# Optimization experiments

Measured on AMD Instinct MI355X. Metric: run time of the kernel, lower is better.

## Reference

```python
import jax, jax.numpy as jnp
import numpy as np

N, E, B = 50000, 400000, 128
F_IN, EDIM, EMB, H = 64, 8, 64, 4
HC = EMB * H  # 256
L = 3          # gnn_layers
DN = 256       # dense_neurons
NEG_SLOPE = 0.2
EPS = 1e-5


def setup_inputs():
    key = jax.random.key(0)
    ks = jax.random.split(key, 32)
    s = 0.05
    d = {}
    d["x"] = jax.random.normal(ks[0], (N, F_IN), jnp.float32)
    d["edge_index"] = jax.random.randint(ks[1], (2, E), 0, N, jnp.int32)
    d["edge_attr"] = jax.random.normal(ks[2], (E, EDIM), jnp.float32)
    d["mol_formal_charge"] = jax.random.normal(ks[3], (B,), jnp.float32)
    d["mol_nrot"] = jax.random.normal(ks[4], (B,), jnp.float32)
    d["batch_index"] = jnp.sort(jax.random.randint(ks[5], (N,), 0, B, jnp.int32))
    # GATv2 params, stacked over L layers (in_dim == EMB == F_IN for all layers)
    d["gat_Wl"] = jax.random.normal(ks[6], (L, F_IN, HC), jnp.float32) * s
    d["gat_Wr"] = jax.random.normal(ks[7], (L, F_IN, HC), jnp.float32) * s
    d["gat_We"] = jax.random.normal(ks[8], (L, EDIM, HC), jnp.float32) * s
    d["gat_att"] = jax.random.normal(ks[9], (L, H, EMB), jnp.float32) * s
    d["gat_b"] = jnp.zeros((L, HC), jnp.float32)
    d["tr_W"] = jax.random.normal(ks[10], (L, HC, EMB), jnp.float32) * s
    d["tr_b"] = jnp.zeros((L, EMB), jnp.float32)
    d["bn_g"] = jnp.ones((L, EMB), jnp.float32)
    d["bn_b"] = jnp.zeros((L, EMB), jnp.float32)
    d["gate_W"] = jax.random.normal(ks[11], (EMB, 1), jnp.float32) * s
    d["gate_b"] = jnp.zeros((1,), jnp.float32)
    d["lin1_W"] = jax.random.normal(ks[12], (EMB + 2, DN), jnp.float32) * s
    d["lin1_b"] = jnp.zeros((DN,), jnp.float32)
    d["fc1_W"] = jax.random.normal(ks[13], (DN, DN // 2), jnp.float32) * s
    d["fc1_b"] = jnp.zeros((DN // 2,), jnp.float32)
    d["fc2_W"] = jax.random.normal(ks[14], (DN // 2, DN // 4), jnp.float32) * s
    d["fc2_b"] = jnp.zeros((DN // 4,), jnp.float32)
    d["out_W"] = jax.random.normal(ks[15], (DN // 4, 1), jnp.float32) * s
    d["out_b"] = jnp.zeros((1,), jnp.float32)
    return d


def _seg_softmax(logits, seg, num):
    # numerically stable per-segment softmax over leading axis
    mx = jax.ops.segment_max(logits, seg, num_segments=num)
    ex = jnp.exp(logits - mx[seg])
    den = jax.ops.segment_sum(ex, seg, num_segments=num)
    return ex / den[seg]


def reference(x, edge_index, edge_attr, mol_formal_charge, mol_nrot, batch_index,
              gat_Wl, gat_Wr, gat_We, gat_att, gat_b, tr_W, tr_b, bn_g, bn_b,
              gate_W, gate_b, lin1_W, lin1_b, fc1_W, fc1_b, fc2_W, fc2_b,
              out_W, out_b):
    src, dst = edge_index[0], edge_index[1]  # messages flow src -> dst
    h = x
    for l in range(L):
        xl = (h @ gat_Wl[l]).reshape(N, H, EMB)
        xr = (h @ gat_Wr[l]).reshape(N, H, EMB)
        ea = (edge_attr @ gat_We[l]).reshape(E, H, EMB)
        xls = xl[src]                                   # [E,H,C]
        m = jax.nn.leaky_relu(xls + xr[dst] + ea, NEG_SLOPE)
        logit = jnp.einsum('ehc,hc->eh', m, gat_att[l])  # [E,H]
        alpha = _seg_softmax(logit, dst, N)              # [E,H]
        agg = jax.ops.segment_sum(alpha[:, :, None] * xls, dst, num_segments=N)
        h = agg.reshape(N, HC) + gat_b[l]
        h = jax.nn.relu(h @ tr_W[l] + tr_b[l])
        # BatchNorm1d (training-mode batch stats, biased var)
        mu = h.mean(0)
        var = h.var(0)
        h = (h - mu) / jnp.sqrt(var + EPS) * bn_g[l] + bn_b[l]
    # AttentionalAggregation pooling
    gate = h @ gate_W + gate_b                           # [N,1]
    w = _seg_softmax(gate, batch_index, B)
    pooled = jax.ops.segment_sum(w * h, batch_index, num_segments=B)  # [B,EMB]
    z = jnp.concatenate([pooled, mol_formal_charge[:, None], mol_nrot[:, None]], axis=1)
    z = jax.nn.relu(z @ lin1_W + lin1_b)
    z = jax.nn.relu(z @ fc1_W + fc1_b)
    z = jax.nn.relu(z @ fc2_W + fc2_b)
    return z @ out_W + out_b                             # [B,1]
```

## Files before the change

kernel.cpp:

```cpp
#include <hip/hip_runtime.h>

#define NN 50000
#define NE 400000
#define NB 128
#define NINF (-__builtin_inff())

__device__ __forceinline__ float dpp_add16(float x) {
    int v = __float_as_int(x);
    x += __int_as_float(__builtin_amdgcn_update_dpp(0, v, 0xB1, 0xF, 0xF, true));
    v = __float_as_int(x);
    x += __int_as_float(__builtin_amdgcn_update_dpp(0, v, 0x4E, 0xF, 0xF, true));
    v = __float_as_int(x);
    x += __int_as_float(__builtin_amdgcn_update_dpp(0, v, 0x141, 0xF, 0xF, true));
    v = __float_as_int(x);
    x += __int_as_float(__builtin_amdgcn_update_dpp(0, v, 0x140, 0xF, 0xF, true));
    return x;
}

__global__ __launch_bounds__(256) void k_hist(const int* __restrict__ dstv, int* __restrict__ deg) {
    int e = blockIdx.x * 256 + threadIdx.x;
    if (e < NE) atomicAdd(&deg[dstv[e]], 1);
}

__global__ __launch_bounds__(1024) void k_scan(const int* __restrict__ deg, int* __restrict__ rowptr) {
    __shared__ int wsum[16];
    __shared__ int total_s;
    const int tid = threadIdx.x, lane = tid & 63, w = tid >> 6;
    if (tid == 0) rowptr[0] = 0;
    int carry = 0;
    for (int base = 0; base < NN; base += 1024) {
        int i = base + tid;
        int v = (i < NN) ? deg[i] : 0;
        int incl = v;
        #pragma unroll
        for (int off = 1; off < 64; off <<= 1) {
            int t = __shfl_up(incl, off);
            if (lane >= off) incl += t;
        }
        if (lane == 63) wsum[w] = incl;
        __syncthreads();
        if (tid < 16) {
            int s = wsum[tid];
            int si = s;
            #pragma unroll
            for (int off = 1; off < 16; off <<= 1) {
                int t = __shfl_up(si, off, 16);
                if (tid >= off) si += t;
            }
            wsum[tid] = si - s;
            if (tid == 15) total_s = si;
        }
        __syncthreads();
        if (i < NN) rowptr[i + 1] = carry + wsum[w] + incl;
        carry += total_s;
        __syncthreads();
    }
}

__global__ __launch_bounds__(256) void k_scatter(const int* __restrict__ dstv, const int* __restrict__ srcv,
                                                 const float* __restrict__ eattr, const int* __restrict__ rowptr,
                                                 int* __restrict__ cnt, int* __restrict__ eid,
                                                 int* __restrict__ src_perm, float4* __restrict__ ea_perm,
                                                 int use_perm) {
    int e = blockIdx.x * 256 + threadIdx.x;
    if (e < NE) {
        int d = dstv[e];
        int pos = rowptr[d] + atomicAdd(&cnt[d], 1);
        eid[pos] = e;
        if (use_perm) {
            src_perm[pos] = srcv[e];
            ea_perm[(size_t)pos * 2] = ((const float4*)eattr)[e * 2];
            ea_perm[(size_t)pos * 2 + 1] = ((const float4*)eattr)[e * 2 + 1];
        }
    }
}

__global__ __launch_bounds__(256) void k_gemm64(const float* __restrict__ A, const float* __restrict__ Wl,
                                                const float* __restrict__ Wr, float* __restrict__ Cl,
                                                float* __restrict__ Cr, const float* __restrict__ stats,
                                                const float* __restrict__ bg, const float* __restrict__ bb) {
    __shared__ float As[64 * 64];
    __shared__ float Ws[64 * 128];
    __shared__ float sc_s[64], sh_s[64], shW_s[128];
    const int tid = threadIdx.x;
    const int mat = blockIdx.y >> 1, ch = blockIdx.y & 1;
    const float* W = mat ? Wr : Wl;
    float* C = mat ? Cr : Cl;
    const int r0b = blockIdx.x * 64;

    if (stats) {
        if (tid < 64) {
            const float mu = stats[tid] * (1.0f / (float)NN);
            const float var = stats[64 + tid] * (1.0f / (float)NN) - mu * mu;
            const float rstd = rsqrtf(var + 1e-5f);
            const float sc = bg[tid] * rstd;
            sc_s[tid] = sc;
            sh_s[tid] = fmaf(-mu, sc, bb[tid]);
        }
        __syncthreads();
    }
    for (int i = tid; i < 2048; i += 256) {
        const int k = i >> 5, c4 = i & 31;
        float4 v = ((const float4*)W)[k * 64 + ch * 32 + c4];
        if (stats) {
            const float s = sc_s[k];
            v.x *= s; v.y *= s; v.z *= s; v.w *= s;
        }
        ((float4*)Ws)[i] = v;
    }
    for (int i = tid; i < 1024; i += 256) {
        const int r = i >> 4, c4 = i & 15;
        const int rg = (r0b + r < NN) ? (r0b + r) : (NN - 1);
        ((float4*)As)[i] = ((const float4*)A)[rg * 16 + c4];
    }
    if (stats && tid < 128) {
        const float* wc = W + ch * 128 + tid;
        float s = 0.f;
        for (int k = 0; k < 64; ++k) s = fmaf(sh_s[k], wc[k * 256], s);
        shW_s[tid] = s;
    }
    __syncthreads();

    const int cg = tid & 31;
    const int rq = tid >> 5;
    float acc[8][4];
    if (stats) {
        #pragma unroll
        for (int rr = 0; rr < 8; ++rr) {
            acc[rr][0] = shW_s[cg * 4]; acc[rr][1] = shW_s[cg * 4 + 1];
            acc[rr][2] = shW_s[cg * 4 + 2]; acc[rr][3] = shW_s[cg * 4 + 3];
        }
    } else {
        #pragma unroll
        for (int rr = 0; rr < 8; ++rr)
            acc[rr][0] = acc[rr][1] = acc[rr][2] = acc[rr][3] = 0.f;
    }

    for (int kq = 0; kq < 16; ++kq) {
        float4 av[8];
        #pragma unroll
        for (int rr = 0; rr < 8; ++rr)
            av[rr] = ((const float4*)As)[(rq * 8 + rr) * 16 + kq];
        #pragma unroll
        for (int kk = 0; kk < 4; ++kk) {
            const float4 w = *(const float4*)(Ws + ((kq * 4 + kk) << 7) + (cg << 2));
            #pragma unroll
            for (int rr = 0; rr < 8; ++rr) {
                const float a = reinterpret_cast<const float*>(&av[rr])[kk];
                acc[rr][0] = fmaf(a, w.x, acc[rr][0]);
                acc[rr][1] = fmaf(a, w.y, acc[rr][1]);
                acc[rr][2] = fmaf(a, w.z, acc[rr][2]);
                acc[rr][3] = fmaf(a, w.w, acc[rr][3]);
            }
        }
    }
    #pragma unroll
    for (int rr = 0; rr < 8; ++rr) {
        const int r = r0b + rq * 8 + rr;
        if (r < NN)
            *(float4*)(C + (size_t)r * 256 + ch * 128 + cg * 4) =
                make_float4(acc[rr][0], acc[rr][1], acc[rr][2], acc[rr][3]);
    }
}

template <bool PERM>
__global__ __launch_bounds__(256, 4) void k_agg(const float* __restrict__ xl, float* __restrict__ xragg,
                                                const float* __restrict__ att, const float* __restrict__ gatb,
                                                const int* __restrict__ rowptr, const int* __restrict__ eid,
                                                const int* __restrict__ srcv, const float* __restrict__ eattr,
                                                const int* __restrict__ src_perm, const float4* __restrict__ ea_perm,
                                                const float* __restrict__ We) {
    const int lane = threadIdx.x & 63;
    const float4 we0 = ((const float4*)(We + 0 * 256))[lane];
    const float4 we1 = ((const float4*)(We + 1 * 256))[lane];
    const float4 we2 = ((const float4*)(We + 2 * 256))[lane];
    const float4 we3 = ((const float4*)(We + 3 * 256))[lane];
    const float4 we4 = ((const float4*)(We + 4 * 256))[lane];
    const float4 we5 = ((const float4*)(We + 5 * 256))[lane];
    const float4 we6 = ((const float4*)(We + 6 * 256))[lane];
    const float4 we7 = ((const float4*)(We + 7 * 256))[lane];
    const float4 attf = ((const float4*)att)[lane];
    const float4 gbf = ((const float4*)gatb)[lane];
    const int nw = gridDim.x * (blockDim.x >> 6);
    int wid = blockIdx.x * (blockDim.x >> 6) + (threadIdx.x >> 6);

#define LOADE(X, idx)                                                          \
    {                                                                          \
        int s_;                                                                \
        const float4* eap_;                                                    \
        if (PERM) {                                                            \
            s_ = src_perm[idx];                                                \
            eap_ = ea_perm + (size_t)(idx) * 2;                                \
        } else {                                                               \
            const int e_ = eid[idx];                                           \
            s_ = srcv[e_];                                                     \
            eap_ = (const float4*)(eattr + (size_t)e_ * 8);                    \
        }                                                                      \
        X##x = ((const float4*)(xl + (size_t)s_ * 256))[lane];                 \
        X##a = eap_[0];                                                        \
        X##b = eap_[1];                                                        \
    }

#define PROC(X)                                                                \
    {                                                                          \
        float v0 = fmaf(X##a.x, we0.x, xr.x), v1 = fmaf(X##a.x, we0.y, xr.y);  \
        float v2 = fmaf(X##a.x, we0.z, xr.z), v3 = fmaf(X##a.x, we0.w, xr.w);  \
        v0 = fmaf(X##a.y, we1.x, v0); v1 = fmaf(X##a.y, we1.y, v1);            \
        v2 = fmaf(X##a.y, we1.z, v2); v3 = fmaf(X##a.y, we1.w, v3);            \
        v0 = fmaf(X##a.z, we2.x, v0); v1 = fmaf(X##a.z, we2.y, v1);            \
        v2 = fmaf(X##a.z, we2.z, v2); v3 = fmaf(X##a.z, we2.w, v3);            \
        v0 = fmaf(X##a.w, we3.x, v0); v1 = fmaf(X##a.w, we3.y, v1);            \
        v2 = fmaf(X##a.w, we3.z, v2); v3 = fmaf(X##a.w, we3.w, v3);            \
        v0 = fmaf(X##b.x, we4.x, v0); v1 = fmaf(X##b.x, we4.y, v1);            \
        v2 = fmaf(X##b.x, we4.z, v2); v3 = fmaf(X##b.x, we4.w, v3);            \
        v0 = fmaf(X##b.y, we5.x, v0); v1 = fmaf(X##b.y, we5.y, v1);            \
        v2 = fmaf(X##b.y, we5.z, v2); v3 = fmaf(X##b.y, we5.w, v3);            \
        v0 = fmaf(X##b.z, we6.x, v0); v1 = fmaf(X##b.z, we6.y, v1);            \
        v2 = fmaf(X##b.z, we6.z, v2); v3 = fmaf(X##b.z, we6.w, v3);            \
        v0 = fmaf(X##b.w, we7.x, v0); v1 = fmaf(X##b.w, we7.y, v1);            \
        v2 = fmaf(X##b.w, we7.z, v2); v3 = fmaf(X##b.w, we7.w, v3);            \
        v0 += X##x.x; v1 += X##x.y; v2 += X##x.z; v3 += X##x.w;                \
        v0 = fmaxf(v0, 0.2f * v0); v1 = fmaxf(v1, 0.2f * v1);                  \
        v2 = fmaxf(v2, 0.2f * v2); v3 = fmaxf(v3, 0.2f * v3);                  \
        float part = v0 * attf.x;                                              \
        part = fmaf(v1, attf.y, part);                                         \
        part = fmaf(v2, attf.z, part);                                         \
        part = fmaf(v3, attf.w, part);                                         \
        part = dpp_add16(part);                                                \
        const float p = __expf(part);                                          \
        den += p;                                                              \
        c0 = fmaf(p, X##x.x, c0);                                              \
        c1 = fmaf(p, X##x.y, c1);                                              \
        c2 = fmaf(p, X##x.z, c2);                                              \
        c3 = fmaf(p, X##x.w, c3);                                              \
    }

    for (int n = wid; n < NN; n += nw) {
        const int e0 = rowptr[n], e1 = rowptr[n + 1];
        const float4 xr = ((const float4*)(xragg + (size_t)n * 256))[lane];
        float den = 0.f, c0 = 0.f, c1 = 0.f, c2 = 0.f, c3 = 0.f;
        float4 Ax, Aa, Ab, Bx, Ba, Bb;
        const int cnt = e1 - e0;
        if (cnt > 0) {
            LOADE(A, e0);
            if (cnt > 1) {
                LOADE(B, e0 + 1);
                int i = e0;
                for (; i + 3 < e1; i += 2) {
                    PROC(A);
                    LOADE(A, i + 2);
                    PROC(B);
                    LOADE(B, i + 3);
                }
                const int r = e1 - i;
                PROC(A);
                if (r == 3) {
                    LOADE(A, i + 2);
                    PROC(B);
                    PROC(A);
                } else {
                    PROC(B);
                }
            } else {
                PROC(A);
            }
        }
        float4 o;
        if (cnt > 0) {
            const float inv = 1.0f / den;
            o.x = fmaf(c0, inv, gbf.x);
            o.y = fmaf(c1, inv, gbf.y);
            o.z = fmaf(c2, inv, gbf.z);
            o.w = fmaf(c3, inv, gbf.w);
        } else {
            o = gbf;
        }
        ((float4*)(xragg + (size_t)n * 256))[lane] = o;
    }
#undef LOADE
#undef PROC
}

__global__ __launch_bounds__(256) void k_tr(const float* __restrict__ A, const float* __restrict__ W,
                                            const float* __restrict__ bias, float* __restrict__ Hout,
                                            float* __restrict__ stats) {
    __shared__ float As[64 * 68];
    __shared__ float Ws[64 * 64];
    __shared__ float red[128];
    const int tid = threadIdx.x;
    const int cg = tid & 15;
    const int rq = tid >> 4;
    const int r0b = blockIdx.x * 64;

    float acc[4][4];
    {
        const float b0 = bias[cg * 4], b1 = bias[cg * 4 + 1], b2 = bias[cg * 4 + 2], b3 = bias[cg * 4 + 3];
        #pragma unroll
        for (int rr = 0; rr < 4; ++rr) { acc[rr][0] = b0; acc[rr][1] = b1; acc[rr][2] = b2; acc[rr][3] = b3; }
    }

    for (int kc = 0; kc < 4; ++kc) {
        if (kc) __syncthreads();
        for (int i = tid; i < 1024; i += 256)
            ((float4*)Ws)[i] = ((const float4*)(W + kc * 4096))[i];
        for (int i = tid; i < 1024; i += 256) {
            const int r = i >> 4, c4 = i & 15;
            const int rg = (r0b + r < NN) ? (r0b + r) : (NN - 1);
            *(float4*)(As + r * 68 + c4 * 4) = ((const float4*)A)[(size_t)rg * 64 + kc * 16 + c4];
        }
        __syncthreads();
        for (int kq = 0; kq < 16; ++kq) {
            float4 av[4];
            #pragma unroll
            for (int rr = 0; rr < 4; ++rr)
                av[rr] = *(const float4*)(As + (rq * 4 + rr) * 68 + kq * 4);
            #pragma unroll
            for (int kk = 0; kk < 4; ++kk) {
                const float4 w = *(const float4*)(Ws + ((kq * 4 + kk) << 6) + (cg << 2));
                #pragma unroll
                for (int rr = 0; rr < 4; ++rr) {
                    const float a = reinterpret_cast<const float*>(&av[rr])[kk];
                    acc[rr][0] = fmaf(a, w.x, acc[rr][0]);
                    acc[rr][1] = fmaf(a, w.y, acc[rr][1]);
                    acc[rr][2] = fmaf(a, w.z, acc[rr][2]);
                    acc[rr][3] = fmaf(a, w.w, acc[rr][3]);
                }
            }
        }
    }
    float lsum[4] = {0.f, 0.f, 0.f, 0.f}, lsq[4] = {0.f, 0.f, 0.f, 0.f};
    #pragma unroll
    for (int rr = 0; rr < 4; ++rr) {
        const int r = r0b + rq * 4 + rr;
        if (r < NN) {
            float v0 = fmaxf(acc[rr][0], 0.f), v1 = fmaxf(acc[rr][1], 0.f);
            float v2 = fmaxf(acc[rr][2], 0.f), v3 = fmaxf(acc[rr][3], 0.f);
            lsum[0] += v0; lsum[1] += v1; lsum[2] += v2; lsum[3] += v3;
            lsq[0] = fmaf(v0, v0, lsq[0]); lsq[1] = fmaf(v1, v1, lsq[1]);
            lsq[2] = fmaf(v2, v2, lsq[2]); lsq[3] = fmaf(v3, v3, lsq[3]);
            *(float4*)(Hout + (size_t)r * 64 + cg * 4) = make_float4(v0, v1, v2, v3);
        }
    }
    __syncthreads();
    if (tid < 128) red[tid] = 0.f;
    __syncthreads();
    #pragma unroll
    for (int j = 0; j < 4; ++j) {
        atomicAdd(&red[cg * 4 + j], lsum[j]);
        atomicAdd(&red[64 + cg * 4 + j], lsq[j]);
    }
    __syncthreads();
    if (tid < 64) {
        atomicAdd(&stats[tid], red[tid]);
        atomicAdd(&stats[64 + tid], red[64 + tid]);
    }
}

__global__ __launch_bounds__(256) void k_poolhead(const float* __restrict__ h, const float* __restrict__ gw,
                                                  const int* __restrict__ bidx, const float* __restrict__ stats,
                                                  const float* __restrict__ bg, const float* __restrict__ bb,
                                                  const float* __restrict__ fc, const float* __restrict__ nrot,
                                                  const float* __restrict__ W1, const float* __restrict__ b1,
                                                  const float* __restrict__ W2, const float* __restrict__ b2,
                                                  const float* __restrict__ W3, const float* __restrict__ b3,
                                                  const float* __restrict__ W4, const float* __restrict__ b4,
                                                  float* __restrict__ out) {
    __shared__ float gate_s[1024];
    __shared__ float red[4];
    __shared__ float pp[4][64];
    __shared__ float scb[64], shb[64];
    __shared__ float z[66], a1[256], a2[128], a3[64];
    const int b = blockIdx.x, tid = threadIdx.x, lane = tid & 63, w = tid >> 6;
    if (tid < 64) {
        const float mu = stats[tid] * (1.0f / (float)NN);
        const float var = stats[64 + tid] * (1.0f / (float)NN) - mu * mu;
        const float rstd = rsqrtf(var + 1e-5f);
        const float sc = bg[tid] * rstd;
        scb[tid] = sc;
        shb[tid] = fmaf(-mu, sc, bb[tid]);
    }
    int lo = 0, hi = NN;
    while (lo < hi) { int mid = (lo + hi) >> 1; if (bidx[mid] < b) lo = mid + 1; else hi = mid; }
    const int s0 = lo;
    lo = 0; hi = NN;
    while (lo < hi) { int mid = (lo + hi) >> 1; if (bidx[mid] < b + 1) lo = mid + 1; else hi = mid; }
    const int s1 = lo;
    const int seg = s1 - s0;
    __syncthreads();

    const float gwv = gw[lane] * scb[lane];
    for (int i = s0 + w; i < s1; i += 4) {
        float p = h[(size_t)i * 64 + lane] * gwv;
        #pragma unroll
        for (int off = 32; off; off >>= 1) p += __shfl_xor(p, off);
        if (lane == 0) gate_s[i - s0] = p;
    }
    __syncthreads();
    float v = NINF;
    for (int i = tid; i < seg; i += 256) v = fmaxf(v, gate_s[i]);
    #pragma unroll
    for (int off = 32; off; off >>= 1) v = fmaxf(v, __shfl_xor(v, off));
    if (lane == 0) red[w] = v;
    __syncthreads();
    const float mx = fmaxf(fmaxf(red[0], red[1]), fmaxf(red[2], red[3]));
    __syncthreads();
    float d = 0.f;
    for (int i = tid; i < seg; i += 256) {
        const float ex = __expf(gate_s[i] - mx);
        gate_s[i] = ex;
        d += ex;
    }
    #pragma unroll
    for (int off = 32; off; off >>= 1) d += __shfl_xor(d, off);
    if (lane == 0) red[w] = d;
    __syncthreads();
    const float den = red[0] + red[1] + red[2] + red[3];
    const int c = tid & 63, ro = tid >> 6;
    float acc = 0.f;
    for (int i = s0 + ro; i < s1; i += 4) acc = fmaf(gate_s[i - s0], h[(size_t)i * 64 + c], acc);
    pp[ro][c] = acc;
    __syncthreads();
    if (tid < 64) {
        const float raw = (pp[0][tid] + pp[1][tid] + pp[2][tid] + pp[3][tid]) / den;
        z[tid] = (seg > 0) ? fmaf(raw, scb[tid], shb[tid]) : shb[tid];
    }
    if (tid == 64) z[64] = fc[b];
    if (tid == 65) z[65] = nrot[b];
    __syncthreads();
    float s = b1[tid];
    for (int k = 0; k < 66; ++k) s = fmaf(z[k], W1[k * 256 + tid], s);
    a1[tid] = fmaxf(s, 0.f);
    __syncthreads();
    if (tid < 128) {
        float s2 = b2[tid];
        for (int k = 0; k < 256; ++k) s2 = fmaf(a1[k], W2[k * 128 + tid], s2);
        a2[tid] = fmaxf(s2, 0.f);
    }
    __syncthreads();
    if (tid < 64) {
        float s3 = b3[tid];
        for (int k = 0; k < 128; ++k) s3 = fmaf(a2[k], W3[k * 64 + tid], s3);
        a3[tid] = fmaxf(s3, 0.f);
    }
    __syncthreads();
    if (tid < 64) {
        float p = a3[tid] * W4[tid];
        #pragma unroll
        for (int off = 32; off; off >>= 1) p += __shfl_xor(p, off);
        if (tid == 0) out[b] = p + b4[0];
    }
}

extern "C" void kernel_launch(void* const* d_in, const int* in_sizes, int n_in,
                              void* d_out, int out_size, void* d_ws, size_t ws_size,
                              hipStream_t stream) {
    const float* x     = (const float*)d_in[0];
    const int*   ei    = (const int*)d_in[1];
    const float* eattr = (const float*)d_in[2];
    const float* fcv   = (const float*)d_in[3];
    const float* nrot  = (const float*)d_in[4];
    const int*   bidx  = (const int*)d_in[5];
    const float* Wl    = (const float*)d_in[6];
    const float* Wr    = (const float*)d_in[7];
    const float* We    = (const float*)d_in[8];
    const float* att   = (const float*)d_in[9];
    const float* gatb  = (const float*)d_in[10];
    const float* trW   = (const float*)d_in[11];
    const float* trb   = (const float*)d_in[12];
    const float* bng   = (const float*)d_in[13];
    const float* bnb   = (const float*)d_in[14];
    const float* gateW = (const float*)d_in[15];
    const float* W1    = (const float*)d_in[17];
    const float* b1    = (const float*)d_in[18];
    const float* W2    = (const float*)d_in[19];
    const float* b2    = (const float*)d_in[20];
    const float* W3    = (const float*)d_in[21];
    const float* b3    = (const float*)d_in[22];
    const float* W4    = (const float*)d_in[23];
    const float* b4    = (const float*)d_in[24];
    float* out = (float*)d_out;

    const int* srcv = ei;
    const int* dstv = ei + NE;

    char* w = (char*)d_ws;
    float*  xl       = (float*)(w);
    float*  xragg    = (float*)(w + 51200000);
    float*  hbuf     = (float*)(w + 102400000);
    int*    deg      = (int*)  (w + 102400000);
    int*    cnt      = (int*)  (w + 102600000);
    int*    eid      = (int*)  (w + 115200000);
    int*    rowptr   = (int*)  (w + 116800000);
    float*  stats    = (float*)(w + 117000064);
    int*    src_perm = (int*)  (w + 117042048);
    float4* ea_perm  = (float4*)(w + 118642048);
    const bool use_perm = (ws_size >= (size_t)131442048);

    hipMemsetAsync(deg, 0, 400000, stream);
    hipMemsetAsync(stats, 0, 1536, stream);
    k_hist<<<(NE + 255) / 256, 256, 0, stream>>>(dstv, deg);
    k_scan<<<1, 1024, 0, stream>>>(deg, rowptr);
    k_scatter<<<(NE + 255) / 256, 256, 0, stream>>>(dstv, srcv, eattr, rowptr, cnt, eid,
                                                    src_perm, ea_perm, use_perm ? 1 : 0);

    const float* hin = x;
    for (int l = 0; l < 3; ++l) {
        const float* st = (l == 0) ? nullptr : (stats + (l - 1) * 128);
        const float* g  = (l == 0) ? nullptr : (bng + (l - 1) * 64);
        const float* bb = (l == 0) ? nullptr : (bnb + (l - 1) * 64);
        dim3 gg((NN + 63) / 64, 4);
        k_gemm64<<<gg, 256, 0, stream>>>(hin, Wl + l * 16384, Wr + l * 16384, xl, xragg, st, g, bb);
        if (use_perm)
            k_agg<true><<<2048, 256, 0, stream>>>(xl, xragg, att + l * 256, gatb + l * 256, rowptr,
                                                  eid, srcv, eattr, src_perm, ea_perm, We + l * 2048);
        else
            k_agg<false><<<2048, 256, 0, stream>>>(xl, xragg, att + l * 256, gatb + l * 256, rowptr,
                                                   eid, srcv, eattr, src_perm, ea_perm, We + l * 2048);
        k_tr<<<(NN + 63) / 64, 256, 0, stream>>>(xragg, trW + l * 16384, trb + l * 64, hbuf, stats + l * 128);
        hin = hbuf;
    }
    k_poolhead<<<NB, 256, 0, stream>>>(hbuf, gateW, bidx, stats + 2 * 128, bng + 128, bnb + 128,
                                       fcv, nrot, W1, b1, W2, b2, W3, b3, W4, b4, out);
}
```

Measured before the change: 759.5 us.

## Parallelize degree scan and enlarge GEMM register tiles with transposed LDS

```diff
diff --git a/kernel.cpp b/kernel.cpp
--- a/kernel.cpp
+++ b/kernel.cpp
@@ -22,39 +22,53 @@
     if (e < NE) atomicAdd(&deg[dstv[e]], 1);
 }
 
-__global__ __launch_bounds__(1024) void k_scan(const int* __restrict__ deg, int* __restrict__ rowptr) {
-    __shared__ int wsum[16];
-    __shared__ int total_s;
+__global__ __launch_bounds__(256) void k_scan1(const int* __restrict__ deg, int* __restrict__ bsum) {
+    __shared__ int ws[4];
     const int tid = threadIdx.x, lane = tid & 63, w = tid >> 6;
-    if (tid == 0) rowptr[0] = 0;
-    int carry = 0;
-    for (int base = 0; base < NN; base += 1024) {
-        int i = base + tid;
-        int v = (i < NN) ? deg[i] : 0;
-        int incl = v;
-        #pragma unroll
-        for (int off = 1; off < 64; off <<= 1) {
-            int t = __shfl_up(incl, off);
-            if (lane >= off) incl += t;
-        }
-        if (lane == 63) wsum[w] = incl;
-        __syncthreads();
-        if (tid < 16) {
-            int s = wsum[tid];
-            int si = s;
-            #pragma unroll
-            for (int off = 1; off < 16; off <<= 1) {
-                int t = __shfl_up(si, off, 16);
-                if (tid >= off) si += t;
-            }
-            wsum[tid] = si - s;
-            if (tid == 15) total_s = si;
-        }
-        __syncthreads();
-        if (i < NN) rowptr[i + 1] = carry + wsum[w] + incl;
-        carry += total_s;
-        __syncthreads();
-    }
+    const int i = blockIdx.x * 256 + tid;
+    int v = (i < NN) ? deg[i] : 0;
+    #pragma unroll
+    for (int off = 32; off; off >>= 1) v += __shfl_xor(v, off);
+    if (lane == 0) ws[w] = v;
+    __syncthreads();
+    if (tid == 0) bsum[blockIdx.x] = ws[0] + ws[1] + ws[2] + ws[3];
+}
+
+__global__ __launch_bounds__(256) void k_scan2(const int* __restrict__ bsum, int* __restrict__ boff, int nblk) {
+    __shared__ int ws[4];
+    const int tid = threadIdx.x, lane = tid & 63, w = tid >> 6;
+    int v = (tid < nblk) ? bsum[tid] : 0;
+    int incl = v;
+    #pragma unroll
+    for (int off = 1; off < 64; off <<= 1) {
+        int t = __shfl_up(incl, off);
+        if (lane >= off) incl += t;
+    }
+    if (lane == 63) ws[w] = incl;
+    __syncthreads();
+    int add = 0;
+    for (int k = 0; k < w; ++k) add += ws[k];
+    if (tid < nblk) boff[tid] = add + incl - v;
+}
+
+__global__ __launch_bounds__(256) void k_scan3(const int* __restrict__ deg, const int* __restrict__ boff,
+                                               int* __restrict__ rowptr) {
+    __shared__ int ws[4];
+    const int tid = threadIdx.x, lane = tid & 63, w = tid >> 6;
+    const int i = blockIdx.x * 256 + tid;
+    int v = (i < NN) ? deg[i] : 0;
+    int incl = v;
+    #pragma unroll
+    for (int off = 1; off < 64; off <<= 1) {
+        int t = __shfl_up(incl, off);
+        if (lane >= off) incl += t;
+    }
+    if (lane == 63) ws[w] = incl;
+    __syncthreads();
+    int add = boff[blockIdx.x];
+    for (int k = 0; k < w; ++k) add += ws[k];
+    if (i < NN) rowptr[i + 1] = add + incl;
+    if (i == 0) rowptr[0] = 0;
 }
 
 __global__ __launch_bounds__(256) void k_scatter(const int* __restrict__ dstv, const int* __restrict__ srcv,
@@ -79,14 +93,14 @@
                                                 const float* __restrict__ Wr, float* __restrict__ Cl,
                                                 float* __restrict__ Cr, const float* __restrict__ stats,
                                                 const float* __restrict__ bg, const float* __restrict__ bb) {
-    __shared__ float As[64 * 64];
+    __shared__ float At[64 * 132];
     __shared__ float Ws[64 * 128];
     __shared__ float sc_s[64], sh_s[64], shW_s[128];
     const int tid = threadIdx.x;
     const int mat = blockIdx.y >> 1, ch = blockIdx.y & 1;
     const float* W = mat ? Wr : Wl;
     float* C = mat ? Cr : Cl;
-    const int r0b = blockIdx.x * 64;
+    const int r0b = blockIdx.x * 128;
 
     if (stats) {
         if (tid < 64) {
@@ -108,10 +122,14 @@
         }
         ((float4*)Ws)[i] = v;
     }
-    for (int i = tid; i < 1024; i += 256) {
-        const int r = i >> 4, c4 = i & 15;
+    for (int i = tid; i < 2048; i += 256) {
+        const int r = i >> 4, kq = i & 15;
         const int rg = (r0b + r < NN) ? (r0b + r) : (NN - 1);
-        ((float4*)As)[i] = ((const float4*)A)[rg * 16 + c4];
+        const float4 v = ((const float4*)A)[rg * 16 + kq];
+        At[(kq * 4 + 0) * 132 + r] = v.x;
+        At[(kq * 4 + 1) * 132 + r] = v.y;
+        At[(kq * 4 + 2) * 132 + r] = v.z;
+        At[(kq * 4 + 3) * 132 + r] = v.w;
     }
     if (stats && tid < 128) {
         const float* wc = W + ch * 128 + tid;
@@ -121,45 +139,49 @@
     }
     __syncthreads();
 
-    const int cg = tid & 31;
-    const int rq = tid >> 5;
-    float acc[8][4];
+    const int cg = tid & 15;
+    const int rg = tid >> 4;
+    float acc[8][8];
     if (stats) {
         #pragma unroll
-        for (int rr = 0; rr < 8; ++rr) {
-            acc[rr][0] = shW_s[cg * 4]; acc[rr][1] = shW_s[cg * 4 + 1];
-            acc[rr][2] = shW_s[cg * 4 + 2]; acc[rr][3] = shW_s[cg * 4 + 3];
-        }
+        for (int rr = 0; rr < 8; ++rr)
+            #pragma unroll
+            for (int j = 0; j < 8; ++j)
+                acc[rr][j] = (j < 4) ? shW_s[cg * 4 + j] : shW_s[64 + cg * 4 + (j - 4)];
     } else {
         #pragma unroll
         for (int rr = 0; rr < 8; ++rr)
-            acc[rr][0] = acc[rr][1] = acc[rr][2] = acc[rr][3] = 0.f;
-    }
-
-    for (int kq = 0; kq < 16; ++kq) {
-        float4 av[8];
+            #pragma unroll
+            for (int j = 0; j < 8; ++j) acc[rr][j] = 0.f;
+    }
+
+    #pragma unroll 4
+    for (int k = 0; k < 64; ++k) {
+        const float4 a0 = *(const float4*)(At + k * 132 + rg * 8);
+        const float4 a1 = *(const float4*)(At + k * 132 + rg * 8 + 4);
+        const float4 w0 = *(const float4*)(Ws + k * 128 + cg * 4);
+        const float4 w1 = *(const float4*)(Ws + k * 128 + 64 + cg * 4);
+        const float ar[8] = {a0.x, a0.y, a0.z, a0.w, a1.x, a1.y, a1.z, a1.w};
         #pragma unroll
-        for (int rr = 0; rr < 8; ++rr)
-            av[rr] = ((const float4*)As)[(rq * 8 + rr) * 16 + kq];
-        #pragma unroll
-        for (int kk = 0; kk < 4; ++kk) {
-            const float4 w = *(const float4*)(Ws + ((kq * 4 + kk) << 7) + (cg << 2));
-            #pragma unroll
-            for (int rr = 0; rr < 8; ++rr) {
-                const float a = reinterpret_cast<const float*>(&av[rr])[kk];
-                acc[rr][0] = fmaf(a, w.x, acc[rr][0]);
-                acc[rr][1] = fmaf(a, w.y, acc[rr][1]);
-                acc[rr][2] = fmaf(a, w.z, acc[rr][2]);
-                acc[rr][3] = fmaf(a, w.w, acc[rr][3]);
-            }
+        for (int rr = 0; rr < 8; ++rr) {
+            acc[rr][0] = fmaf(ar[rr], w0.x, acc[rr][0]);
+            acc[rr][1] = fmaf(ar[rr], w0.y, acc[rr][1]);
+            acc[rr][2] = fmaf(ar[rr], w0.z, acc[rr][2]);
+            acc[rr][3] = fmaf(ar[rr], w0.w, acc[rr][3]);
+            acc[rr][4] = fmaf(ar[rr], w1.x, acc[rr][4]);
+            acc[rr][5] = fmaf(ar[rr], w1.y, acc[rr][5]);
+            acc[rr][6] = fmaf(ar[rr], w1.z, acc[rr][6]);
+            acc[rr][7] = fmaf(ar[rr], w1.w, acc[rr][7]);
         }
     }
     #pragma unroll
     for (int rr = 0; rr < 8; ++rr) {
-        const int r = r0b + rq * 8 + rr;
-        if (r < NN)
-            *(float4*)(C + (size_t)r * 256 + ch * 128 + cg * 4) =
-                make_float4(acc[rr][0], acc[rr][1], acc[rr][2], acc[rr][3]);
+        const int r = r0b + rg * 8 + rr;
+        if (r < NN) {
+            float* cp = C + (size_t)r * 256 + ch * 128 + cg * 4;
+            *(float4*)cp = make_float4(acc[rr][0], acc[rr][1], acc[rr][2], acc[rr][3]);
+            *(float4*)(cp + 64) = make_float4(acc[rr][4], acc[rr][5], acc[rr][6], acc[rr][7]);
+        }
     }
 }
 
@@ -281,73 +303,85 @@
 #undef PROC
 }
 
-__global__ __launch_bounds__(256) void k_tr(const float* __restrict__ A, const float* __restrict__ W,
+__global__ __launch_bounds__(128) void k_tr(const float* __restrict__ A, const float* __restrict__ W,
                                             const float* __restrict__ bias, float* __restrict__ Hout,
                                             float* __restrict__ stats) {
-    __shared__ float As[64 * 68];
-    __shared__ float Ws[64 * 64];
+    __shared__ float At[32 * 132];
+    __shared__ float Ws[32 * 64];
     __shared__ float red[128];
     const int tid = threadIdx.x;
-    const int cg = tid & 15;
-    const int rq = tid >> 4;
-    const int r0b = blockIdx.x * 64;
-
-    float acc[4][4];
-    {
-        const float b0 = bias[cg * 4], b1 = bias[cg * 4 + 1], b2 = bias[cg * 4 + 2], b3 = bias[cg * 4 + 3];
+    const int cg = tid & 7;
+    const int rg = tid >> 3;
+    const int r0b = blockIdx.x * 128;
+
+    float acc[8][8];
+    #pragma unroll
+    for (int rr = 0; rr < 8; ++rr)
         #pragma unroll
-        for (int rr = 0; rr < 4; ++rr) { acc[rr][0] = b0; acc[rr][1] = b1; acc[rr][2] = b2; acc[rr][3] = b3; }
-    }
-
-    for (int kc = 0; kc < 4; ++kc) {
+        for (int j = 0; j < 8; ++j)
+            acc[rr][j] = bias[(j < 4) ? (cg * 4 + j) : (32 + cg * 4 + (j - 4))];
+
+    for (int kc = 0; kc < 8; ++kc) {
         if (kc) __syncthreads();
-        for (int i = tid; i < 1024; i += 256)
-            ((float4*)Ws)[i] = ((const float4*)(W + kc * 4096))[i];
-        for (int i = tid; i < 1024; i += 256) {
-            const int r = i >> 4, c4 = i & 15;
-            const int rg = (r0b + r < NN) ? (r0b + r) : (NN - 1);
-            *(float4*)(As + r * 68 + c4 * 4) = ((const float4*)A)[(size_t)rg * 64 + kc * 16 + c4];
+        for (int i = tid; i < 512; i += 128)
+            ((float4*)Ws)[i] = ((const float4*)(W + kc * 2048))[i];
+        for (int i = tid; i < 1024; i += 128) {
+            const int r = i >> 3, c4 = i & 7;
+            const int rgl = (r0b + r < NN) ? (r0b + r) : (NN - 1);
+            const float4 v = ((const float4*)A)[(size_t)rgl * 64 + kc * 8 + c4];
+            At[(c4 * 4 + 0) * 132 + r] = v.x;
+            At[(c4 * 4 + 1) * 132 + r] = v.y;
+            At[(c4 * 4 + 2) * 132 + r] = v.z;
+            At[(c4 * 4 + 3) * 132 + r] = v.w;
         }
         __syncthreads();
-        for (int kq = 0; kq < 16; ++kq) {
-            float4 av[4];
+        #pragma unroll 4
+        for (int k = 0; k < 32; ++k) {
+            const float4 a0 = *(const float4*)(At + k * 132 + rg * 8);
+            const float4 a1 = *(const float4*)(At + k * 132 + rg * 8 + 4);
+            const float4 w0 = *(const float4*)(Ws + k * 64 + cg * 4);
+            const float4 w1 = *(const float4*)(Ws + k * 64 + 32 + cg * 4);
+            const float ar[8] = {a0.x, a0.y, a0.z, a0.w, a1.x, a1.y, a1.z, a1.w};
             #pragma unroll
-            for (int rr = 0; rr < 4; ++rr)
-                av[rr] = *(const float4*)(As + (rq * 4 + rr) * 68 + kq * 4);
+            for (int rr = 0; rr < 8; ++rr) {
+                acc[rr][0] = fmaf(ar[rr], w0.x, acc[rr][0]);
+                acc[rr][1] = fmaf(ar[rr], w0.y, acc[rr][1]);
+                acc[rr][2] = fmaf(ar[rr], w0.z, acc[rr][2]);
+                acc[rr][3] = fmaf(ar[rr], w0.w, acc[rr][3]);
+                acc[rr][4] = fmaf(ar[rr], w1.x, acc[rr][4]);
+                acc[rr][5] = fmaf(ar[rr], w1.y, acc[rr][5]);
+                acc[rr][6] = fmaf(ar[rr], w1.z, acc[rr][6]);
+                acc[rr][7] = fmaf(ar[rr], w1.w, acc[rr][7]);
+            }
+        }
+    }
+    float lsum[8], lsq[8];
+    #pragma unroll
+    for (int j = 0; j < 8; ++j) { lsum[j] = 0.f; lsq[j] = 0.f; }
+    #pragma unroll
+    for (int rr = 0; rr < 8; ++rr) {
+        const int r = r0b + rg * 8 + rr;
+        if (r < NN) {
+            float v[8];
             #pragma unroll
-            for (int kk = 0; kk < 4; ++kk) {
-                const float4 w = *(const float4*)(Ws + ((kq * 4 + kk) << 6) + (cg << 2));
-                #pragma unroll
-                for (int rr = 0; rr < 4; ++rr) {
-                    const float a = reinterpret_cast<const float*>(&av[rr])[kk];
-                    acc[rr][0] = fmaf(a, w.x, acc[rr][0]);
-                    acc[rr][1] = fmaf(a, w.y, acc[rr][1]);
-                    acc[rr][2] = fmaf(a, w.z, acc[rr][2]);
-                    acc[rr][3] = fmaf(a, w.w, acc[rr][3]);
-                }
+            for (int j = 0; j < 8; ++j) {
+                v[j] = fmaxf(acc[rr][j], 0.f);
+                lsum[j] += v[j];
+                lsq[j] = fmaf(v[j], v[j], lsq[j]);
             }
-        }
-    }
-    float lsum[4] = {0.f, 0.f, 0.f, 0.f}, lsq[4] = {0.f, 0.f, 0.f, 0.f};
-    #pragma unroll
-    for (int rr = 0; rr < 4; ++rr) {
-        const int r = r0b + rq * 4 + rr;
-        if (r < NN) {
-            float v0 = fmaxf(acc[rr][0], 0.f), v1 = fmaxf(acc[rr][1], 0.f);
-            float v2 = fmaxf(acc[rr][2], 0.f), v3 = fmaxf(acc[rr][3], 0.f);
-            lsum[0] += v0; lsum[1] += v1; lsum[2] += v2; lsum[3] += v3;
-            lsq[0] = fmaf(v0, v0, lsq[0]); lsq[1] = fmaf(v1, v1, lsq[1]);
-            lsq[2] = fmaf(v2, v2, lsq[2]); lsq[3] = fmaf(v3, v3, lsq[3]);
-            *(float4*)(Hout + (size_t)r * 64 + cg * 4) = make_float4(v0, v1, v2, v3);
-        }
-    }
-    __syncthreads();
-    if (tid < 128) red[tid] = 0.f;
-    __syncthreads();
-    #pragma unroll
-    for (int j = 0; j < 4; ++j) {
-        atomicAdd(&red[cg * 4 + j], lsum[j]);
-        atomicAdd(&red[64 + cg * 4 + j], lsq[j]);
+            float* hp = Hout + (size_t)r * 64;
+            *(float4*)(hp + cg * 4) = make_float4(v[0], v[1], v[2], v[3]);
+            *(float4*)(hp + 32 + cg * 4) = make_float4(v[4], v[5], v[6], v[7]);
+        }
+    }
+    __syncthreads();
+    red[tid] = 0.f;
+    __syncthreads();
+    #pragma unroll
+    for (int j = 0; j < 8; ++j) {
+        const int c = (j < 4) ? (cg * 4 + j) : (32 + cg * 4 + (j - 4));
+        atomicAdd(&red[c], lsum[j]);
+        atomicAdd(&red[64 + c], lsq[j]);
     }
     __syncthreads();
     if (tid < 64) {
@@ -492,14 +526,19 @@
     int*    eid      = (int*)  (w + 115200000);
     int*    rowptr   = (int*)  (w + 116800000);
     float*  stats    = (float*)(w + 117000064);
+    int*    bsum     = (int*)  (w + 117004096);
+    int*    boff     = (int*)  (w + 117006144);
     int*    src_perm = (int*)  (w + 117042048);
     float4* ea_perm  = (float4*)(w + 118642048);
     const bool use_perm = (ws_size >= (size_t)131442048);
+    const int NBLK = (NN + 255) / 256;
 
     hipMemsetAsync(deg, 0, 400000, stream);
     hipMemsetAsync(stats, 0, 1536, stream);
     k_hist<<<(NE + 255) / 256, 256, 0, stream>>>(dstv, deg);
-    k_scan<<<1, 1024, 0, stream>>>(deg, rowptr);
+    k_scan1<<<NBLK, 256, 0, stream>>>(deg, bsum);
+    k_scan2<<<1, 256, 0, stream>>>(bsum, boff, NBLK);
+    k_scan3<<<NBLK, 256, 0, stream>>>(deg, boff, rowptr);
     k_scatter<<<(NE + 255) / 256, 256, 0, stream>>>(dstv, srcv, eattr, rowptr, cnt, eid,
                                                     src_perm, ea_perm, use_perm ? 1 : 0);
 
@@ -508,7 +547,7 @@
         const float* st = (l == 0) ? nullptr : (stats + (l - 1) * 128);
         const float* g  = (l == 0) ? nullptr : (bng + (l - 1) * 64);
         const float* bb = (l == 0) ? nullptr : (bnb + (l - 1) * 64);
-        dim3 gg((NN + 63) / 64, 4);
+        dim3 gg((NN + 127) / 128, 4);
         k_gemm64<<<gg, 256, 0, stream>>>(hin, Wl + l * 16384, Wr + l * 16384, xl, xragg, st, g, bb);
         if (use_perm)
             k_agg<true><<<2048, 256, 0, stream>>>(xl, xragg, att + l * 256, gatb + l * 256, rowptr,
@@ -516,7 +555,7 @@
         else
             k_agg<false><<<2048, 256, 0, stream>>>(xl, xragg, att + l * 256, gatb + l * 256, rowptr,
                                                    eid, srcv, eattr, src_perm, ea_perm, We + l * 2048);
-        k_tr<<<(NN + 63) / 64, 256, 0, stream>>>(xragg, trW + l * 16384, trb + l * 64, hbuf, stats + l * 128);
+        k_tr<<<(NN + 127) / 128, 128, 0, stream>>>(xragg, trW + l * 16384, trb + l * 64, hbuf, stats + l * 128);
         hin = hbuf;
     }
     k_poolhead<<<NB, 256, 0, stream>>>(hbuf, gateW, bidx, stats + 2 * 128, bng + 128, bnb + 128,
```

After: 754.7 us. No clear change (-0.6%).
